# Optimization experiments

Measured on AMD Instinct MI355X. Metric: run time of the kernel, lower is better.

Reference implementation:

```python
import jax, jax.numpy as jnp
import numpy as np

EMB = 512
HEADS = 8
HEAD_DIM = EMB // HEADS


def setup_inputs() -> dict:
    key = jax.random.key(0)
    ks = jax.random.split(key, 9)
    s = 1.0 / np.sqrt(EMB)
    return {
        "x": jax.random.normal(ks[0], (4, 2048, EMB), dtype=jnp.float32),
        "Wq": jax.random.uniform(ks[1], (EMB, EMB), jnp.float32, -s, s),
        "bq": jax.random.uniform(ks[2], (EMB,), jnp.float32, -s, s),
        "Wk": jax.random.uniform(ks[3], (EMB, EMB), jnp.float32, -s, s),
        "bk": jax.random.uniform(ks[4], (EMB,), jnp.float32, -s, s),
        "Wv": jax.random.uniform(ks[5], (EMB, EMB), jnp.float32, -s, s),
        "bv": jax.random.uniform(ks[6], (EMB,), jnp.float32, -s, s),
        "Wp": jax.random.uniform(ks[7], (EMB, EMB), jnp.float32, -s, s),
        "bp": jax.random.uniform(ks[8], (EMB,), jnp.float32, -s, s),
    }


def _split_heads(t):
    b, n, _ = t.shape
    return t.reshape(b, n, HEADS, HEAD_DIM).transpose(0, 2, 1, 3)  # b h n d


def reference(x, Wq, bq, Wk, bk, Wv, bv, Wp, bp):
    q = _split_heads(x @ Wq.T + bq)
    k = _split_heads(x @ Wk.T + bk)
    v = _split_heads(x @ Wv.T + bv)
    energy = jnp.einsum("bhqd,bhkd->bhqk", q, k)
    # NOTE: original applies softmax to UNSCALED logits, then divides probs by sqrt(emb)
    att = jax.nn.softmax(energy, axis=-1) / jnp.sqrt(jnp.float32(EMB))
    out = jnp.einsum("bhqk,bhkd->bhqd", att, v)
    b, h, n, d = out.shape
    out = out.transpose(0, 2, 1, 3).reshape(b, n, h * d)
    return out @ Wp.T + bp
```

## Files before the change

### kernel.cpp

```cpp
#include <hip/hip_runtime.h>
#include <math.h>
#include <stdint.h>

#define SEQ  2048
#define LOG2E 1.4426950408889634f

typedef __attribute__((ext_vector_type(4))) float f32x4;
typedef __attribute__((ext_vector_type(16))) float f32x16;
typedef __attribute__((ext_vector_type(8))) short bf16x8;

template <int V> struct IC { static constexpr int value = V; };

__device__ __forceinline__ unsigned packbf(float a, float b) {
    return __builtin_amdgcn_perm(__float_as_uint(b) + 0x8000u,
                                 __float_as_uint(a) + 0x8000u, 0x07060302u);
}

__global__ __launch_bounds__(256) void cvt_kernel(
    const float* __restrict__ x,  const float* __restrict__ wq,
    const float* __restrict__ wk, const float* __restrict__ wv,
    const float* __restrict__ wp,
    unsigned short* __restrict__ xb,  unsigned short* __restrict__ wqb,
    unsigned short* __restrict__ wkb, unsigned short* __restrict__ wvb,
    unsigned short* __restrict__ wpb)
{
    const int c = blockIdx.x * 256 + threadIdx.x;
    const float* s;
    unsigned short* d;
    int off;
    if (c < 524288) {
        s = x; d = xb; off = c;
    } else {
        const int cc = c - 524288;
        const int wsel = cc >> 15;
        off = cc & 32767;
        s = wsel == 0 ? wq : wsel == 1 ? wk : wsel == 2 ? wv : wp;
        d = wsel == 0 ? wqb : wsel == 1 ? wkb : wsel == 2 ? wvb : wpb;
    }
    const float4* sp = (const float4*)s + (size_t)off * 2;
    const float4 a = sp[0], b = sp[1];
    uint4 p;
    p.x = packbf(a.x, a.y); p.y = packbf(a.z, a.w);
    p.z = packbf(b.x, b.y); p.w = packbf(b.z, b.w);
    *((uint4*)d + off) = p;
}

__global__ __launch_bounds__(256, 3) void qkv_kernel(
    const unsigned short* __restrict__ xb, const unsigned short* __restrict__ wqb,
    const unsigned short* __restrict__ wkb, const unsigned short* __restrict__ wvb,
    const float* __restrict__ bq, const float* __restrict__ bk,
    const float* __restrict__ bv,
    unsigned short* __restrict__ Qw, unsigned short* __restrict__ Kw,
    unsigned short* __restrict__ VTw)
{
    __shared__ __align__(16) unsigned short smem[16384];
    unsigned short* As = smem;
    unsigned short* Bs = smem + 8192;

    const int t = threadIdx.x;
    const int w = t >> 6, lane = t & 63, quad = (t >> 4) & 3, l15 = t & 15;
    const int wr = w >> 1, wc = w & 1;
    const int m0 = blockIdx.y * 128;
    const int n0 = blockIdx.x * 128;
    const int which = n0 >> 9;
    const unsigned short* wbase = which == 0 ? wqb : (which == 1 ? wkb : wvb);
    const int nrow = n0 & 511;

    const int ar = t >> 2, ac = t & 3;
    const unsigned short* ax = xb + (size_t)(m0 + ar) * 512 + ac * 8;
    const unsigned short* bx = wbase + (size_t)(nrow + ar) * 512 + ac * 8;
    const int lws = (ar & 15) | (ac << 4);
    const int off0 = (ar >> 4) * 512 + lws * 8;

    f32x4 acc[4][4];
#pragma unroll
    for (int mt = 0; mt < 4; ++mt)
#pragma unroll
        for (int nt = 0; nt < 4; ++nt) acc[mt][nt] = (f32x4){0.f, 0.f, 0.f, 0.f};

    uint4 ra0, ra1, ra2, ra3, rb0, rb1, rb2, rb3;
    auto loadt = [&](int k0) {
        ra0 = *(const uint4*)(ax + k0);
        ra1 = *(const uint4*)(ax + k0 + 32);
        ra2 = *(const uint4*)(ax + 32768 + k0);
        ra3 = *(const uint4*)(ax + 32768 + k0 + 32);
        rb0 = *(const uint4*)(bx + k0);
        rb1 = *(const uint4*)(bx + k0 + 32);
        rb2 = *(const uint4*)(bx + 32768 + k0);
        rb3 = *(const uint4*)(bx + 32768 + k0 + 32);
    };
    auto writet = [&]() {
        *(uint4*)(As + off0) = ra0;
        *(uint4*)(As + off0 + 4096) = ra1;
        *(uint4*)(As + off0 + 2048) = ra2;
        *(uint4*)(As + off0 + 2048 + 4096) = ra3;
        *(uint4*)(Bs + off0) = rb0;
        *(uint4*)(Bs + off0 + 4096) = rb1;
        *(uint4*)(Bs + off0 + 2048) = rb2;
        *(uint4*)(Bs + off0 + 2048 + 4096) = rb3;
    };

    loadt(0);
    auto kloop = [&](auto TRC) {
        constexpr int TR = decltype(TRC)::value;
        for (int ki = 0; ki < 8; ++ki) {
            writet();
            if (ki < 7) loadt((ki + 1) * 64);
            __syncthreads();
#pragma unroll
            for (int s = 0; s < 2; ++s) {
                bf16x8 af[4], bfr[4];
#pragma unroll
                for (int mt = 0; mt < 4; ++mt)
                    af[mt] = *(const bf16x8*)(As + s * 4096 +
                                              ((wr * 4 + mt) * 64 + lane) * 8);
#pragma unroll
                for (int nt = 0; nt < 4; ++nt)
                    bfr[nt] = *(const bf16x8*)(Bs + s * 4096 +
                                               ((wc * 4 + nt) * 64 + lane) * 8);
#pragma unroll
                for (int mt = 0; mt < 4; ++mt)
#pragma unroll
                    for (int nt = 0; nt < 4; ++nt) {
                        if (TR)
                            acc[mt][nt] = __builtin_amdgcn_mfma_f32_16x16x32_bf16(
                                bfr[nt], af[mt], acc[mt][nt], 0, 0, 0);
                        else
                            acc[mt][nt] = __builtin_amdgcn_mfma_f32_16x16x32_bf16(
                                af[mt], bfr[nt], acc[mt][nt], 0, 0, 0);
                    }
            }
            if (ki < 7) __syncthreads();
        }
    };
    if (which < 2) kloop(IC<1>{});
    else           kloop(IC<0>{});

    if (which == 2) {
#pragma unroll
        for (int nt = 0; nt < 4; ++nt) {
            const int n = n0 + wc * 64 + nt * 16 + l15;
            const float bias = bv[n & 511];
            const int h = (n >> 6) & 7, d = n & 63;
#pragma unroll
            for (int mt = 0; mt < 4; ++mt) {
                const int mb = m0 + wr * 64 + mt * 16 + quad * 4;
                const int bi = mb >> 11, ns = mb & 2047;
                const int bhl = bi * 8 + h;
                const f32x4 v = acc[mt][nt];
                uint2 pk;
                pk.x = packbf(v[0] + bias, v[1] + bias);
                pk.y = packbf(v[2] + bias, v[3] + bias);
                const size_t off =
                    ((size_t)(bhl * 32 + (ns >> 6)) * 8 + ((d >> 5) << 2) +
                     ((ns >> 4) & 3)) * 512 +
                    ((d & 31) << 3) + ((ns & 8) << 5) + (ns & 7);
                *(uint2*)(VTw + off) = pk;
            }
        }
    } else {
        const float sc = which ? 1.f : LOG2E;
        const float* bpt = which ? bk : bq;
        unsigned short* base = which ? Kw : Qw;
#pragma unroll
        for (int nt = 0; nt < 4; ++nt) {
            const int nb = n0 + wc * 64 + nt * 16 + quad * 4;
            const f32x4 bvv = *(const f32x4*)(bpt + (nb & 511));
            const int h = (nb >> 6) & 7, d0 = nb & 63;
#pragma unroll
            for (int mt = 0; mt < 4; ++mt) {
                const int nsg = m0 + wr * 64 + mt * 16 + l15;
                const int bi = nsg >> 11, ns = nsg & 2047;
                const int bhl = bi * 8 + h;
                const f32x4 v = acc[mt][nt];
                uint2 pk;
                pk.x = packbf((v[0] + bvv[0]) * sc, (v[1] + bvv[1]) * sc);
                pk.y = packbf((v[2] + bvv[2]) * sc, (v[3] + bvv[3]) * sc);
                const size_t off =
                    ((size_t)(bhl * 64 + (ns >> 5)) * 4 + (d0 >> 4)) * 512 +
                    ((d0 & 8) << 5) + ((ns & 31) << 3) + (d0 & 7);
                *(uint2*)(base + off) = pk;
            }
        }
    }
}

__global__ __launch_bounds__(256, 3) void outproj_kernel(
    const unsigned short* __restrict__ Aw, const unsigned short* __restrict__ wpb,
    const float* __restrict__ bp, float* __restrict__ out)
{
    __shared__ __align__(16) unsigned short smem[16384];
    unsigned short* As = smem;
    unsigned short* Bs = smem + 8192;

    const int t = threadIdx.x;
    const int w = t >> 6, lane = t & 63, quad = (t >> 4) & 3, l15 = t & 15;
    const int wr = w >> 1, wc = w & 1;
    const int m0 = blockIdx.y * 128;
    const int n0 = blockIdx.x * 128;

    const int ar = t >> 2, ac = t & 3;
    const unsigned short* ap = Aw + (size_t)(m0 + ar) * 512 + ac * 8;
    const unsigned short* bx = wpb + (size_t)(n0 + ar) * 512 + ac * 8;
    const int lws = (ar & 15) | (ac << 4);
    const int off0 = (ar >> 4) * 512 + lws * 8;

    f32x4 acc[4][4];
#pragma unroll
    for (int mt = 0; mt < 4; ++mt)
#pragma unroll
        for (int nt = 0; nt < 4; ++nt) acc[mt][nt] = (f32x4){0.f, 0.f, 0.f, 0.f};

    uint4 ra0, ra1, ra2, ra3, rb0, rb1, rb2, rb3;
    auto loadt = [&](int k0) {
        ra0 = *(const uint4*)(ap + k0);
        ra1 = *(const uint4*)(ap + k0 + 32);
        ra2 = *(const uint4*)(ap + 32768 + k0);
        ra3 = *(const uint4*)(ap + 32768 + k0 + 32);
        rb0 = *(const uint4*)(bx + k0);
        rb1 = *(const uint4*)(bx + k0 + 32);
        rb2 = *(const uint4*)(bx + 32768 + k0);
        rb3 = *(const uint4*)(bx + 32768 + k0 + 32);
    };
    auto writet = [&]() {
        *(uint4*)(As + off0) = ra0;
        *(uint4*)(As + off0 + 4096) = ra1;
        *(uint4*)(As + off0 + 2048) = ra2;
        *(uint4*)(As + off0 + 2048 + 4096) = ra3;
        *(uint4*)(Bs + off0) = rb0;
        *(uint4*)(Bs + off0 + 4096) = rb1;
        *(uint4*)(Bs + off0 + 2048) = rb2;
        *(uint4*)(Bs + off0 + 2048 + 4096) = rb3;
    };

    loadt(0);
    for (int ki = 0; ki < 8; ++ki) {
        writet();
        if (ki < 7) loadt((ki + 1) * 64);
        __syncthreads();
#pragma unroll
        for (int s = 0; s < 2; ++s) {
            bf16x8 af[4], bfr[4];
#pragma unroll
            for (int mt = 0; mt < 4; ++mt)
                af[mt] = *(const bf16x8*)(As + s * 4096 +
                                          ((wr * 4 + mt) * 64 + lane) * 8);
#pragma unroll
            for (int nt = 0; nt < 4; ++nt)
                bfr[nt] = *(const bf16x8*)(Bs + s * 4096 +
                                           ((wc * 4 + nt) * 64 + lane) * 8);
#pragma unroll
            for (int mt = 0; mt < 4; ++mt)
#pragma unroll
                for (int nt = 0; nt < 4; ++nt)
                    acc[mt][nt] = __builtin_amdgcn_mfma_f32_16x16x32_bf16(
                        af[mt], bfr[nt], acc[mt][nt], 0, 0, 0);
        }
        if (ki < 7) __syncthreads();
    }

#pragma unroll
    for (int nt = 0; nt < 4; ++nt) {
        const int n = n0 + wc * 64 + nt * 16 + l15;
        const float bias = bp[n];
#pragma unroll
        for (int mt = 0; mt < 4; ++mt) {
            const int mb = m0 + wr * 64 + mt * 16 + quad * 4;
            const f32x4 v = acc[mt][nt];
#pragma unroll
            for (int r = 0; r < 4; ++r)
                out[(size_t)(mb + r) * 512 + n] = v[r] + bias;
        }
    }
}

#define ATTN_STEP(STC, STN, JT)                                                \
    do {                                                                       \
        const int jt_ = (JT);                                                  \
        bf16x8 vc[4];                                                          \
        _Pragma("unroll")                                                      \
        for (int dg = 0; dg < 2; ++dg)                                         \
            _Pragma("unroll")                                                  \
            for (int p = 0; p < 2; ++p)                                        \
                vc[dg * 2 + p] = *(const bf16x8*)(                             \
                    Vp + (size_t)jt_ * 4096 + (dg * 4 + jh * 2 + p) * 512);    \
        STN = zero;                                                            \
        __builtin_amdgcn_s_setprio(1);                                         \
        _Pragma("unroll")                                                      \
        for (int kt = 0; kt < 4; ++kt)                                         \
            STN = __builtin_amdgcn_mfma_f32_32x32x16_bf16(kc[kt], qf[kt],      \
                                                          STN, 0, 0, 0);       \
        __builtin_amdgcn_s_setprio(0);                                         \
        const int jn_ = (jt_ < 30) ? jt_ + 2 : 31;                             \
        _Pragma("unroll")                                                      \
        for (int c = 0; c < 4; ++c)                                            \
            kc[c] = *(const bf16x8*)(Kp + (size_t)jn_ * 4096 + c * 512);       \
        _Pragma("unroll")                                                      \
        for (int r = 0; r < 16; ++r)                                           \
            STC[r] = __builtin_amdgcn_exp2f(STC[r]);                           \
        {                                                                      \
            float s01 = STC[0] + STC[1],   s23 = STC[2] + STC[3];              \
            float s45 = STC[4] + STC[5],   s67 = STC[6] + STC[7];              \
            float s89 = STC[8] + STC[9],   sAB = STC[10] + STC[11];            \
            float sCD = STC[12] + STC[13], sEF = STC[14] + STC[15];            \
            lpart += ((s01 + s23) + (s45 + s67)) + ((s89 + sAB) + (sCD + sEF));\
        }                                                                      \
        _Pragma("unroll")                                                      \
        for (int p = 0; p < 2; ++p) {                                          \
            const int r0 = p * 8;                                              \
            unsigned a0, a1, b0, b1;                                           \
            asm("v_cvt_pk_bf16_f32 %0, %1, %2"                                 \
                : "=v"(a0) : "v"(STC[r0 + 0]), "v"(STC[r0 + 1]));              \
            asm("v_cvt_pk_bf16_f32 %0, %1, %2"                                 \
                : "=v"(a1) : "v"(STC[r0 + 2]), "v"(STC[r0 + 3]));              \
            asm("v_cvt_pk_bf16_f32 %0, %1, %2"                                 \
                : "=v"(b0) : "v"(STC[r0 + 4]), "v"(STC[r0 + 5]));              \
            asm("v_cvt_pk_bf16_f32 %0, %1, %2"                                 \
                : "=v"(b1) : "v"(STC[r0 + 6]), "v"(STC[r0 + 7]));              \
            asm("v_permlane32_swap_b32 %0, %1" : "+v"(a0), "+v"(b0));          \
            asm("v_permlane32_swap_b32 %0, %1" : "+v"(a1), "+v"(b1));          \
            union { unsigned u[4]; bf16x8 v; } pb;                             \
            pb.u[0] = a0;                                                      \
            pb.u[1] = a1;                                                      \
            pb.u[2] = b0;                                                      \
            pb.u[3] = b1;                                                      \
            __builtin_amdgcn_s_setprio(1);                                     \
            Ot[0] = __builtin_amdgcn_mfma_f32_32x32x16_bf16(vc[0 + p], pb.v,   \
                                                            Ot[0], 0, 0, 0);   \
            Ot[1] = __builtin_amdgcn_mfma_f32_32x32x16_bf16(vc[2 + p], pb.v,   \
                                                            Ot[1], 0, 0, 0);   \
            __builtin_amdgcn_s_setprio(0);                                     \
        }                                                                      \
    } while (0)

__global__ __launch_bounds__(512, 2) void attn_kernel(
    const unsigned short* __restrict__ Qf, const unsigned short* __restrict__ Kf,
    const unsigned short* __restrict__ Vf, unsigned short* __restrict__ Ow)
{
    __shared__ float cb[8448];
    const int t = threadIdx.x;
    const int w = t >> 6, lane = t & 63;
    const int l31 = lane & 31, hlf = lane >> 5;
    const int qi = w >> 1, jh = w & 1;

    if (w & 4) __builtin_amdgcn_s_sleep(15);

    const int bh = blockIdx.x;
    const int qblk = blockIdx.y;
    const int q0 = qblk * 128;

    const unsigned short* Kp = Kf + (size_t)bh * 131072 + (jh * 4) * 512 + lane * 8;
    const unsigned short* Vp = Vf + (size_t)bh * 131072 + lane * 8;

    const int qgg = qblk * 4 + qi;
    const unsigned short* Qp = Qf + ((size_t)(bh * 64 + qgg) * 4) * 512 + lane * 8;
    bf16x8 qf[4];
#pragma unroll
    for (int kt = 0; kt < 4; ++kt)
        qf[kt] = *(const bf16x8*)(Qp + kt * 512);

    f32x16 zero;
#pragma unroll
    for (int r = 0; r < 16; ++r) zero[r] = 0.f;

    float lpart = 0.f;
    f32x16 Ot[2];
    Ot[0] = zero; Ot[1] = zero;

    bf16x8 kc[4];
#pragma unroll
    for (int c = 0; c < 4; ++c)
        kc[c] = *(const bf16x8*)(Kp + c * 512);

    f32x16 stA = zero, stB = zero;
#pragma unroll
    for (int kt = 0; kt < 4; ++kt)
        stA = __builtin_amdgcn_mfma_f32_32x32x16_bf16(kc[kt], qf[kt], stA, 0, 0, 0);
#pragma unroll
    for (int c = 0; c < 4; ++c)
        kc[c] = *(const bf16x8*)(Kp + 4096 + c * 512);

    for (int jt = 0; jt < 32; jt += 2) {
        ATTN_STEP(stA, stB, jt);
        ATTN_STEP(stB, stA, jt + 1);
    }

    if (jh == 1) {
#pragma unroll
        for (int dg = 0; dg < 2; ++dg) {
            const int cidx = (qi * 2 + dg) * 4;
#pragma unroll
            for (int k = 0; k < 4; ++k) {
                float4 v = make_float4(
                    Ot[dg][k * 4 + 0], Ot[dg][k * 4 + 1],
                    Ot[dg][k * 4 + 2], Ot[dg][k * 4 + 3]);
                *(float4*)(cb + (cidx + k) * 256 + lane * 4) = v;
            }
        }
        cb[8192 + qi * 64 + lane] = lpart;
    }
    __syncthreads();
    if (jh == 0) {
        const int bi = bh >> 3, h = bh & 7;
#pragma unroll
        for (int dg = 0; dg < 2; ++dg) {
            const int cidx = (qi * 2 + dg) * 4;
#pragma unroll
            for (int k = 0; k < 4; ++k) {
                const float4 v = *(const float4*)(cb + (cidx + k) * 256 + lane * 4);
                Ot[dg][k * 4 + 0] += v.x;
                Ot[dg][k * 4 + 1] += v.y;
                Ot[dg][k * 4 + 2] += v.z;
                Ot[dg][k * 4 + 3] += v.w;
            }
        }
        float lv = lpart + cb[8192 + qi * 64 + lane];
        lv += __shfl_xor(lv, 32);
        const float inv = 1.0f / (lv * 22.627416997969522f);

        const int ns = q0 + qi * 32 + l31;
        unsigned short* dst = Ow + ((size_t)bi * SEQ + ns) * 512 + h * 64 + hlf * 4;
#pragma unroll
        for (int dg = 0; dg < 2; ++dg)
#pragma unroll
            for (int rb2 = 0; rb2 < 4; ++rb2) {
                uint2 pk;
                pk.x = packbf(Ot[dg][rb2 * 4 + 0] * inv,
                              Ot[dg][rb2 * 4 + 1] * inv);
                pk.y = packbf(Ot[dg][rb2 * 4 + 2] * inv,
                              Ot[dg][rb2 * 4 + 3] * inv);
                *(uint2*)(dst + dg * 32 + rb2 * 8) = pk;
            }
    }
}

extern "C" void kernel_launch(void* const* d_in, const int* in_sizes, int n_in,
                              void* d_out, int out_size, void* d_ws, size_t ws_size,
                              hipStream_t stream)
{
    const float* x  = (const float*)d_in[0];
    const float* Wq = (const float*)d_in[1];
    const float* bq = (const float*)d_in[2];
    const float* Wk = (const float*)d_in[3];
    const float* bk = (const float*)d_in[4];
    const float* Wv = (const float*)d_in[5];
    const float* bv = (const float*)d_in[6];
    const float* Wp = (const float*)d_in[7];
    const float* bp = (const float*)d_in[8];

    unsigned short* ws = (unsigned short*)d_ws;
    unsigned short* Qw  = ws;
    unsigned short* Kw  = Qw + 4194304;
    unsigned short* VTw = Kw + 4194304;
    unsigned short* Owb = VTw + 4194304;
    unsigned short* xb  = Owb;
    unsigned short* wqb = Owb + 4194304;
    unsigned short* wkb = wqb + 262144;
    unsigned short* wvb = wkb + 262144;
    unsigned short* wpb = wvb + 262144;

    cvt_kernel<<<dim3(2560), 256, 0, stream>>>(
        x, Wq, Wk, Wv, Wp, xb, wqb, wkb, wvb, wpb);
    qkv_kernel<<<dim3(12, 64), 256, 0, stream>>>(
        xb, wqb, wkb, wvb, bq, bk, bv, Qw, Kw, VTw);
    attn_kernel<<<dim3(32, 16), 512, 0, stream>>>(Qw, Kw, VTw, Owb);
    outproj_kernel<<<dim3(4, 64), 256, 0, stream>>>(Owb, wpb, bp, (float*)d_out);
}
```

Before: 162.9 us.

## Use direct global-to-LDS loads in QKV GEMM and drop attention wave sleep

The QKV projection now stages A and B tiles with global_load_lds (16-byte direct-to-LDS loads) instead of loading into registers and then writing to shared memory. The K step is halved to 32 and LDS use shrinks to 16KB. The register-prefetch software pipelining is gone, so each iteration now waits on its own load before computing, which exposes load latency. Separately, the s_sleep stagger for the upper waves in the attention kernel is removed.

New measurement: 164.7 us. No clear change (+1.1%).

```diff
diff --git a/kernel.cpp b/kernel.cpp
--- a/kernel.cpp
+++ b/kernel.cpp
@@ -14,6 +14,12 @@
 __device__ __forceinline__ unsigned packbf(float a, float b) {
     return __builtin_amdgcn_perm(__float_as_uint(b) + 0x8000u,
                                  __float_as_uint(a) + 0x8000u, 0x07060302u);
+}
+
+__device__ __forceinline__ void gload16(const unsigned short* g, unsigned short* l) {
+    __builtin_amdgcn_global_load_lds(
+        (const __attribute__((address_space(1))) unsigned int*)g,
+        (__attribute__((address_space(3))) unsigned int*)l, 16, 0, 0);
 }
 
 __global__ __launch_bounds__(256) void cvt_kernel(
@@ -53,9 +59,9 @@
     unsigned short* __restrict__ Qw, unsigned short* __restrict__ Kw,
     unsigned short* __restrict__ VTw)
 {
-    __shared__ __align__(16) unsigned short smem[16384];
+    __shared__ __align__(16) unsigned short smem[8192];
     unsigned short* As = smem;
-    unsigned short* Bs = smem + 8192;
+    unsigned short* Bs = smem + 4096;
 
     const int t = threadIdx.x;
     const int w = t >> 6, lane = t & 63, quad = (t >> 4) & 3, l15 = t & 15;
@@ -66,11 +72,8 @@
     const unsigned short* wbase = which == 0 ? wqb : (which == 1 ? wkb : wvb);
     const int nrow = n0 & 511;
 
-    const int ar = t >> 2, ac = t & 3;
-    const unsigned short* ax = xb + (size_t)(m0 + ar) * 512 + ac * 8;
-    const unsigned short* bx = wbase + (size_t)(nrow + ar) * 512 + ac * 8;
-    const int lws = (ar & 15) | (ac << 4);
-    const int off0 = (ar >> 4) * 512 + lws * 8;
+    const unsigned short* axg = xb + (size_t)(m0 + w * 16 + (lane & 15)) * 512 + ((lane >> 4) * 8);
+    const unsigned short* bxg = wbase + (size_t)(nrow + w * 16 + (lane & 15)) * 512 + ((lane >> 4) * 8);
 
     f32x4 acc[4][4];
 #pragma unroll
@@ -78,59 +81,39 @@
 #pragma unroll
         for (int nt = 0; nt < 4; ++nt) acc[mt][nt] = (f32x4){0.f, 0.f, 0.f, 0.f};
 
-    uint4 ra0, ra1, ra2, ra3, rb0, rb1, rb2, rb3;
-    auto loadt = [&](int k0) {
-        ra0 = *(const uint4*)(ax + k0);
-        ra1 = *(const uint4*)(ax + k0 + 32);
-        ra2 = *(const uint4*)(ax + 32768 + k0);
-        ra3 = *(const uint4*)(ax + 32768 + k0 + 32);
-        rb0 = *(const uint4*)(bx + k0);
-        rb1 = *(const uint4*)(bx + k0 + 32);
-        rb2 = *(const uint4*)(bx + 32768 + k0);
-        rb3 = *(const uint4*)(bx + 32768 + k0 + 32);
+    auto stage = [&](int k0) {
+        unsigned short* Ad = As + w * 512;
+        unsigned short* Bd = Bs + w * 512;
+        gload16(axg + k0, Ad);
+        gload16(axg + 32768 + k0, Ad + 2048);
+        gload16(bxg + k0, Bd);
+        gload16(bxg + 32768 + k0, Bd + 2048);
     };
-    auto writet = [&]() {
-        *(uint4*)(As + off0) = ra0;
-        *(uint4*)(As + off0 + 4096) = ra1;
-        *(uint4*)(As + off0 + 2048) = ra2;
-        *(uint4*)(As + off0 + 2048 + 4096) = ra3;
-        *(uint4*)(Bs + off0) = rb0;
-        *(uint4*)(Bs + off0 + 4096) = rb1;
-        *(uint4*)(Bs + off0 + 2048) = rb2;
-        *(uint4*)(Bs + off0 + 2048 + 4096) = rb3;
-    };
-
-    loadt(0);
+
     auto kloop = [&](auto TRC) {
         constexpr int TR = decltype(TRC)::value;
-        for (int ki = 0; ki < 8; ++ki) {
-            writet();
-            if (ki < 7) loadt((ki + 1) * 64);
+        for (int ki = 0; ki < 16; ++ki) {
+            stage(ki * 32);
             __syncthreads();
-#pragma unroll
-            for (int s = 0; s < 2; ++s) {
-                bf16x8 af[4], bfr[4];
-#pragma unroll
-                for (int mt = 0; mt < 4; ++mt)
-                    af[mt] = *(const bf16x8*)(As + s * 4096 +
-                                              ((wr * 4 + mt) * 64 + lane) * 8);
-#pragma unroll
-                for (int nt = 0; nt < 4; ++nt)
-                    bfr[nt] = *(const bf16x8*)(Bs + s * 4096 +
-                                               ((wc * 4 + nt) * 64 + lane) * 8);
-#pragma unroll
-                for (int mt = 0; mt < 4; ++mt)
-#pragma unroll
-                    for (int nt = 0; nt < 4; ++nt) {
-                        if (TR)
-                            acc[mt][nt] = __builtin_amdgcn_mfma_f32_16x16x32_bf16(
-                                bfr[nt], af[mt], acc[mt][nt], 0, 0, 0);
-                        else
-                            acc[mt][nt] = __builtin_amdgcn_mfma_f32_16x16x32_bf16(
-                                af[mt], bfr[nt], acc[mt][nt], 0, 0, 0);
-                    }
-            }
-            if (ki < 7) __syncthreads();
+            bf16x8 af[4], bfr[4];
+#pragma unroll
+            for (int mt = 0; mt < 4; ++mt)
+                af[mt] = *(const bf16x8*)(As + ((wr * 4 + mt) * 64 + lane) * 8);
+#pragma unroll
+            for (int nt = 0; nt < 4; ++nt)
+                bfr[nt] = *(const bf16x8*)(Bs + ((wc * 4 + nt) * 64 + lane) * 8);
+#pragma unroll
+            for (int mt = 0; mt < 4; ++mt)
+#pragma unroll
+                for (int nt = 0; nt < 4; ++nt) {
+                    if (TR)
+                        acc[mt][nt] = __builtin_amdgcn_mfma_f32_16x16x32_bf16(
+                            bfr[nt], af[mt], acc[mt][nt], 0, 0, 0);
+                    else
+                        acc[mt][nt] = __builtin_amdgcn_mfma_f32_16x16x32_bf16(
+                            af[mt], bfr[nt], acc[mt][nt], 0, 0, 0);
+                }
+            if (ki < 15) __syncthreads();
         }
     };
     if (which < 2) kloop(IC<1>{});
@@ -343,8 +326,6 @@
     const int l31 = lane & 31, hlf = lane >> 5;
     const int qi = w >> 1, jh = w & 1;
 
-    if (w & 4) __builtin_amdgcn_s_sleep(15);
-
     const int bh = blockIdx.x;
     const int qblk = blockIdx.y;
     const int q0 = qblk * 128;
```

## Stage K/V tiles in LDS via async global_load_lds double buffering

Applied to the files above, without the earlier changes.

The attention loop now cooperatively loads each K/V tile into shared memory with global_load_lds into a double buffer, and every wave reads its fragments from LDS. Before, each wave loaded K and V straight from global memory into registers with a software-pipelined ping-pong of score tiles. This shares loads across the waves of a block, which cuts redundant global traffic and drops the staggered-sleep trick. In exchange it adds a block-wide barrier every tile, removes the overlap of the next QK MFMA with the current exp, and reuses the reduction buffer as the K/V staging area.

After: 159.8 us (median of 2 runs). Within noise of the previous version (-1.9%).

```diff
diff --git a/kernel.cpp b/kernel.cpp
--- a/kernel.cpp
+++ b/kernel.cpp
@@ -14,6 +14,12 @@
 __device__ __forceinline__ unsigned packbf(float a, float b) {
     return __builtin_amdgcn_perm(__float_as_uint(b) + 0x8000u,
                                  __float_as_uint(a) + 0x8000u, 0x07060302u);
+}
+
+__device__ __forceinline__ void gload16(const unsigned short* g, unsigned short* l) {
+    __builtin_amdgcn_global_load_lds(
+        (const __attribute__((address_space(1))) unsigned int*)g,
+        (__attribute__((address_space(3))) unsigned int*)l, 16, 0, 0);
 }
 
 __global__ __launch_bounds__(256) void cvt_kernel(
@@ -274,83 +280,24 @@
     }
 }
 
-#define ATTN_STEP(STC, STN, JT)                                                \
-    do {                                                                       \
-        const int jt_ = (JT);                                                  \
-        bf16x8 vc[4];                                                          \
-        _Pragma("unroll")                                                      \
-        for (int dg = 0; dg < 2; ++dg)                                         \
-            _Pragma("unroll")                                                  \
-            for (int p = 0; p < 2; ++p)                                        \
-                vc[dg * 2 + p] = *(const bf16x8*)(                             \
-                    Vp + (size_t)jt_ * 4096 + (dg * 4 + jh * 2 + p) * 512);    \
-        STN = zero;                                                            \
-        __builtin_amdgcn_s_setprio(1);                                         \
-        _Pragma("unroll")                                                      \
-        for (int kt = 0; kt < 4; ++kt)                                         \
-            STN = __builtin_amdgcn_mfma_f32_32x32x16_bf16(kc[kt], qf[kt],      \
-                                                          STN, 0, 0, 0);       \
-        __builtin_amdgcn_s_setprio(0);                                         \
-        const int jn_ = (jt_ < 30) ? jt_ + 2 : 31;                             \
-        _Pragma("unroll")                                                      \
-        for (int c = 0; c < 4; ++c)                                            \
-            kc[c] = *(const bf16x8*)(Kp + (size_t)jn_ * 4096 + c * 512);       \
-        _Pragma("unroll")                                                      \
-        for (int r = 0; r < 16; ++r)                                           \
-            STC[r] = __builtin_amdgcn_exp2f(STC[r]);                           \
-        {                                                                      \
-            float s01 = STC[0] + STC[1],   s23 = STC[2] + STC[3];              \
-            float s45 = STC[4] + STC[5],   s67 = STC[6] + STC[7];              \
-            float s89 = STC[8] + STC[9],   sAB = STC[10] + STC[11];            \
-            float sCD = STC[12] + STC[13], sEF = STC[14] + STC[15];            \
-            lpart += ((s01 + s23) + (s45 + s67)) + ((s89 + sAB) + (sCD + sEF));\
-        }                                                                      \
-        _Pragma("unroll")                                                      \
-        for (int p = 0; p < 2; ++p) {                                          \
-            const int r0 = p * 8;                                              \
-            unsigned a0, a1, b0, b1;                                           \
-            asm("v_cvt_pk_bf16_f32 %0, %1, %2"                                 \
-                : "=v"(a0) : "v"(STC[r0 + 0]), "v"(STC[r0 + 1]));              \
-            asm("v_cvt_pk_bf16_f32 %0, %1, %2"                                 \
-                : "=v"(a1) : "v"(STC[r0 + 2]), "v"(STC[r0 + 3]));              \
-            asm("v_cvt_pk_bf16_f32 %0, %1, %2"                                 \
-                : "=v"(b0) : "v"(STC[r0 + 4]), "v"(STC[r0 + 5]));              \
-            asm("v_cvt_pk_bf16_f32 %0, %1, %2"                                 \
-                : "=v"(b1) : "v"(STC[r0 + 6]), "v"(STC[r0 + 7]));              \
-            asm("v_permlane32_swap_b32 %0, %1" : "+v"(a0), "+v"(b0));          \
-            asm("v_permlane32_swap_b32 %0, %1" : "+v"(a1), "+v"(b1));          \
-            union { unsigned u[4]; bf16x8 v; } pb;                             \
-            pb.u[0] = a0;                                                      \
-            pb.u[1] = a1;                                                      \
-            pb.u[2] = b0;                                                      \
-            pb.u[3] = b1;                                                      \
-            __builtin_amdgcn_s_setprio(1);                                     \
-            Ot[0] = __builtin_amdgcn_mfma_f32_32x32x16_bf16(vc[0 + p], pb.v,   \
-                                                            Ot[0], 0, 0, 0);   \
-            Ot[1] = __builtin_amdgcn_mfma_f32_32x32x16_bf16(vc[2 + p], pb.v,   \
-                                                            Ot[1], 0, 0, 0);   \
-            __builtin_amdgcn_s_setprio(0);                                     \
-        }                                                                      \
-    } while (0)
-
 __global__ __launch_bounds__(512, 2) void attn_kernel(
     const unsigned short* __restrict__ Qf, const unsigned short* __restrict__ Kf,
     const unsigned short* __restrict__ Vf, unsigned short* __restrict__ Ow)
 {
-    __shared__ float cb[8448];
+    __shared__ __align__(16) float cb[8448];
+    unsigned short* kv = (unsigned short*)cb;
+
     const int t = threadIdx.x;
     const int w = t >> 6, lane = t & 63;
     const int l31 = lane & 31, hlf = lane >> 5;
     const int qi = w >> 1, jh = w & 1;
 
-    if (w & 4) __builtin_amdgcn_s_sleep(15);
-
     const int bh = blockIdx.x;
     const int qblk = blockIdx.y;
     const int q0 = qblk * 128;
 
-    const unsigned short* Kp = Kf + (size_t)bh * 131072 + (jh * 4) * 512 + lane * 8;
-    const unsigned short* Vp = Vf + (size_t)bh * 131072 + lane * 8;
+    const unsigned short* Kt = Kf + (size_t)bh * 131072;
+    const unsigned short* Vt = Vf + (size_t)bh * 131072;
 
     const int qgg = qblk * 4 + qi;
     const unsigned short* Qp = Qf + ((size_t)(bh * 64 + qgg) * 4) * 512 + lane * 8;
@@ -367,22 +314,76 @@
     f32x16 Ot[2];
     Ot[0] = zero; Ot[1] = zero;
 
-    bf16x8 kc[4];
-#pragma unroll
-    for (int c = 0; c < 4; ++c)
-        kc[c] = *(const bf16x8*)(Kp + c * 512);
-
-    f32x16 stA = zero, stB = zero;
-#pragma unroll
-    for (int kt = 0; kt < 4; ++kt)
-        stA = __builtin_amdgcn_mfma_f32_32x32x16_bf16(kc[kt], qf[kt], stA, 0, 0, 0);
-#pragma unroll
-    for (int c = 0; c < 4; ++c)
-        kc[c] = *(const bf16x8*)(Kp + 4096 + c * 512);
-
-    for (int jt = 0; jt < 32; jt += 2) {
-        ATTN_STEP(stA, stB, jt);
-        ATTN_STEP(stB, stA, jt + 1);
+    auto stage = [&](int b, int jt) {
+        unsigned short* dst = kv + b * 8192 + w * 512;
+        gload16(Kt + (size_t)jt * 4096 + w * 512 + lane * 8, dst);
+        gload16(Vt + (size_t)jt * 4096 + w * 512 + lane * 8, dst + 4096);
+    };
+
+    stage(0, 0);
+    __syncthreads();
+    int cur = 0;
+
+    for (int jt = 0; jt < 32; ++jt) {
+        if (jt < 31) stage(cur ^ 1, jt + 1);
+
+        const unsigned short* kb = kv + cur * 8192;
+        bf16x8 kc[4], vc[4];
+#pragma unroll
+        for (int c = 0; c < 4; ++c)
+            kc[c] = *(const bf16x8*)(kb + (jh * 4 + c) * 512 + lane * 8);
+#pragma unroll
+        for (int dg = 0; dg < 2; ++dg)
+#pragma unroll
+            for (int p = 0; p < 2; ++p)
+                vc[dg * 2 + p] = *(const bf16x8*)(
+                    kb + 4096 + (dg * 4 + jh * 2 + p) * 512 + lane * 8);
+
+        f32x16 st = zero;
+        __builtin_amdgcn_s_setprio(1);
+#pragma unroll
+        for (int kt = 0; kt < 4; ++kt)
+            st = __builtin_amdgcn_mfma_f32_32x32x16_bf16(kc[kt], qf[kt], st, 0, 0, 0);
+        __builtin_amdgcn_s_setprio(0);
+
+#pragma unroll
+        for (int r = 0; r < 16; ++r)
+            st[r] = __builtin_amdgcn_exp2f(st[r]);
+        {
+            float s01 = st[0] + st[1],   s23 = st[2] + st[3];
+            float s45 = st[4] + st[5],   s67 = st[6] + st[7];
+            float s89 = st[8] + st[9],   sAB = st[10] + st[11];
+            float sCD = st[12] + st[13], sEF = st[14] + st[15];
+            lpart += ((s01 + s23) + (s45 + s67)) + ((s89 + sAB) + (sCD + sEF));
+        }
+
+#pragma unroll
+        for (int p = 0; p < 2; ++p) {
+            const int r0 = p * 8;
+            unsigned a0, a1, b0, b1;
+            asm("v_cvt_pk_bf16_f32 %0, %1, %2"
+                : "=v"(a0) : "v"(st[r0 + 0]), "v"(st[r0 + 1]));
+            asm("v_cvt_pk_bf16_f32 %0, %1, %2"
+                : "=v"(a1) : "v"(st[r0 + 2]), "v"(st[r0 + 3]));
+            asm("v_cvt_pk_bf16_f32 %0, %1, %2"
+                : "=v"(b0) : "v"(st[r0 + 4]), "v"(st[r0 + 5]));
+            asm("v_cvt_pk_bf16_f32 %0, %1, %2"
+                : "=v"(b1) : "v"(st[r0 + 6]), "v"(st[r0 + 7]));
+            asm("v_permlane32_swap_b32 %0, %1" : "+v"(a0), "+v"(b0));
+            asm("v_permlane32_swap_b32 %0, %1" : "+v"(a1), "+v"(b1));
+            union { unsigned u[4]; bf16x8 v; } pb;
+            pb.u[0] = a0;
+            pb.u[1] = a1;
+            pb.u[2] = b0;
+            pb.u[3] = b1;
+            __builtin_amdgcn_s_setprio(1);
+            Ot[0] = __builtin_amdgcn_mfma_f32_32x32x16_bf16(vc[0 + p], pb.v, Ot[0], 0, 0, 0);
+            Ot[1] = __builtin_amdgcn_mfma_f32_32x32x16_bf16(vc[2 + p], pb.v, Ot[1], 0, 0, 0);
+            __builtin_amdgcn_s_setprio(0);
+        }
+
+        __syncthreads();
+        cur ^= 1;
     }
 
     if (jh == 1) {
```

## Stage K/V tiles into LDS via async global_load_lds double buffering

Applied to the files above, without the earlier changes.

Replaces per-wave direct global loads of K and V fragments with cooperative asynchronous global-to-LDS copies into a double-buffered shared tile, two key tiles per iteration. All eight waves share each staged tile instead of every wave fetching its own K/V from global or L2, which cuts redundant global traffic. The software-pipelined QK/softmax interleave and the staggered s_sleep for half the waves are removed. The change adds a __syncthreads per iteration and 64KB of LDS per block, which may limit occupancy at two blocks per CU.

Result: no change. 160.9 us (-1.2%).

```diff
diff --git a/kernel.cpp b/kernel.cpp
--- a/kernel.cpp
+++ b/kernel.cpp
@@ -14,6 +14,12 @@
 __device__ __forceinline__ unsigned packbf(float a, float b) {
     return __builtin_amdgcn_perm(__float_as_uint(b) + 0x8000u,
                                  __float_as_uint(a) + 0x8000u, 0x07060302u);
+}
+
+__device__ __forceinline__ void gload16(const unsigned short* g, unsigned short* l) {
+    __builtin_amdgcn_global_load_lds(
+        (const __attribute__((address_space(1))) unsigned int*)g,
+        (__attribute__((address_space(3))) unsigned int*)l, 16, 0, 0);
 }
 
 __global__ __launch_bounds__(256) void cvt_kernel(
@@ -274,35 +280,23 @@
     }
 }
 
-#define ATTN_STEP(STC, STN, JT)                                                \
+#define ATTN_FINISH(ST, KB)                                                    \
     do {                                                                       \
-        const int jt_ = (JT);                                                  \
         bf16x8 vc[4];                                                          \
         _Pragma("unroll")                                                      \
         for (int dg = 0; dg < 2; ++dg)                                         \
             _Pragma("unroll")                                                  \
             for (int p = 0; p < 2; ++p)                                        \
                 vc[dg * 2 + p] = *(const bf16x8*)(                             \
-                    Vp + (size_t)jt_ * 4096 + (dg * 4 + jh * 2 + p) * 512);    \
-        STN = zero;                                                            \
-        __builtin_amdgcn_s_setprio(1);                                         \
-        _Pragma("unroll")                                                      \
-        for (int kt = 0; kt < 4; ++kt)                                         \
-            STN = __builtin_amdgcn_mfma_f32_32x32x16_bf16(kc[kt], qf[kt],      \
-                                                          STN, 0, 0, 0);       \
-        __builtin_amdgcn_s_setprio(0);                                         \
-        const int jn_ = (jt_ < 30) ? jt_ + 2 : 31;                             \
-        _Pragma("unroll")                                                      \
-        for (int c = 0; c < 4; ++c)                                            \
-            kc[c] = *(const bf16x8*)(Kp + (size_t)jn_ * 4096 + c * 512);       \
+                    (KB) + 4096 + (dg * 4 + jh * 2 + p) * 512 + lane * 8);     \
         _Pragma("unroll")                                                      \
         for (int r = 0; r < 16; ++r)                                           \
-            STC[r] = __builtin_amdgcn_exp2f(STC[r]);                           \
+            ST[r] = __builtin_amdgcn_exp2f(ST[r]);                             \
         {                                                                      \
-            float s01 = STC[0] + STC[1],   s23 = STC[2] + STC[3];              \
-            float s45 = STC[4] + STC[5],   s67 = STC[6] + STC[7];              \
-            float s89 = STC[8] + STC[9],   sAB = STC[10] + STC[11];            \
-            float sCD = STC[12] + STC[13], sEF = STC[14] + STC[15];            \
+            float s01 = ST[0] + ST[1],   s23 = ST[2] + ST[3];                  \
+            float s45 = ST[4] + ST[5],   s67 = ST[6] + ST[7];                  \
+            float s89 = ST[8] + ST[9],   sAB = ST[10] + ST[11];                \
+            float sCD = ST[12] + ST[13], sEF = ST[14] + ST[15];                \
             lpart += ((s01 + s23) + (s45 + s67)) + ((s89 + sAB) + (sCD + sEF));\
         }                                                                      \
         _Pragma("unroll")                                                      \
@@ -310,13 +304,13 @@
             const int r0 = p * 8;                                              \
             unsigned a0, a1, b0, b1;                                           \
             asm("v_cvt_pk_bf16_f32 %0, %1, %2"                                 \
-                : "=v"(a0) : "v"(STC[r0 + 0]), "v"(STC[r0 + 1]));              \
+                : "=v"(a0) : "v"(ST[r0 + 0]), "v"(ST[r0 + 1]));                \
             asm("v_cvt_pk_bf16_f32 %0, %1, %2"                                 \
-                : "=v"(a1) : "v"(STC[r0 + 2]), "v"(STC[r0 + 3]));              \
+                : "=v"(a1) : "v"(ST[r0 + 2]), "v"(ST[r0 + 3]));                \
             asm("v_cvt_pk_bf16_f32 %0, %1, %2"                                 \
-                : "=v"(b0) : "v"(STC[r0 + 4]), "v"(STC[r0 + 5]));              \
+                : "=v"(b0) : "v"(ST[r0 + 4]), "v"(ST[r0 + 5]));                \
             asm("v_cvt_pk_bf16_f32 %0, %1, %2"                                 \
-                : "=v"(b1) : "v"(STC[r0 + 6]), "v"(STC[r0 + 7]));              \
+                : "=v"(b1) : "v"(ST[r0 + 6]), "v"(ST[r0 + 7]));                \
             asm("v_permlane32_swap_b32 %0, %1" : "+v"(a0), "+v"(b0));          \
             asm("v_permlane32_swap_b32 %0, %1" : "+v"(a1), "+v"(b1));          \
             union { unsigned u[4]; bf16x8 v; } pb;                             \
@@ -337,20 +331,21 @@
     const unsigned short* __restrict__ Qf, const unsigned short* __restrict__ Kf,
     const unsigned short* __restrict__ Vf, unsigned short* __restrict__ Ow)
 {
-    __shared__ float cb[8448];
+    __shared__ __align__(16) unsigned short kvs[32768];
+    unsigned short* kv = kvs;
+    float* cb = (float*)kvs;
+
     const int t = threadIdx.x;
     const int w = t >> 6, lane = t & 63;
     const int l31 = lane & 31, hlf = lane >> 5;
     const int qi = w >> 1, jh = w & 1;
 
-    if (w & 4) __builtin_amdgcn_s_sleep(15);
-
     const int bh = blockIdx.x;
     const int qblk = blockIdx.y;
     const int q0 = qblk * 128;
 
-    const unsigned short* Kp = Kf + (size_t)bh * 131072 + (jh * 4) * 512 + lane * 8;
-    const unsigned short* Vp = Vf + (size_t)bh * 131072 + lane * 8;
+    const unsigned short* Kt = Kf + (size_t)bh * 131072;
+    const unsigned short* Vt = Vf + (size_t)bh * 131072;
 
     const int qgg = qblk * 4 + qi;
     const unsigned short* Qp = Qf + ((size_t)(bh * 64 + qgg) * 4) * 512 + lane * 8;
@@ -367,22 +362,49 @@
     f32x16 Ot[2];
     Ot[0] = zero; Ot[1] = zero;
 
-    bf16x8 kc[4];
-#pragma unroll
-    for (int c = 0; c < 4; ++c)
-        kc[c] = *(const bf16x8*)(Kp + c * 512);
-
-    f32x16 stA = zero, stB = zero;
-#pragma unroll
-    for (int kt = 0; kt < 4; ++kt)
-        stA = __builtin_amdgcn_mfma_f32_32x32x16_bf16(kc[kt], qf[kt], stA, 0, 0, 0);
-#pragma unroll
-    for (int c = 0; c < 4; ++c)
-        kc[c] = *(const bf16x8*)(Kp + 4096 + c * 512);
-
-    for (int jt = 0; jt < 32; jt += 2) {
-        ATTN_STEP(stA, stB, jt);
-        ATTN_STEP(stB, stA, jt + 1);
+    auto stage = [&](int b, int slot, int jt) {
+        unsigned short* dst = kv + b * 16384 + slot * 8192 + w * 512;
+        gload16(Kt + (size_t)jt * 4096 + w * 512 + lane * 8, dst);
+        gload16(Vt + (size_t)jt * 4096 + w * 512 + lane * 8, dst + 4096);
+    };
+
+    stage(0, 0, 0);
+    stage(0, 1, 1);
+    __syncthreads();
+    int cur = 0;
+
+    for (int it = 0; it < 16; ++it) {
+        if (it < 15) {
+            stage(cur ^ 1, 0, 2 * it + 2);
+            stage(cur ^ 1, 1, 2 * it + 3);
+        }
+
+        const unsigned short* kb0 = kv + cur * 16384;
+        const unsigned short* kb1 = kb0 + 8192;
+
+        bf16x8 kc0[4], kc1[4];
+#pragma unroll
+        for (int c = 0; c < 4; ++c)
+            kc0[c] = *(const bf16x8*)(kb0 + (jh * 4 + c) * 512 + lane * 8);
+#pragma unroll
+        for (int c = 0; c < 4; ++c)
+            kc1[c] = *(const bf16x8*)(kb1 + (jh * 4 + c) * 512 + lane * 8);
+
+        f32x16 st0 = zero, st1 = zero;
+        __builtin_amdgcn_s_setprio(1);
+#pragma unroll
+        for (int kt = 0; kt < 4; ++kt)
+            st0 = __builtin_amdgcn_mfma_f32_32x32x16_bf16(kc0[kt], qf[kt], st0, 0, 0, 0);
+#pragma unroll
+        for (int kt = 0; kt < 4; ++kt)
+            st1 = __builtin_amdgcn_mfma_f32_32x32x16_bf16(kc1[kt], qf[kt], st1, 0, 0, 0);
+        __builtin_amdgcn_s_setprio(0);
+
+        ATTN_FINISH(st0, kb0);
+        ATTN_FINISH(st1, kb1);
+
+        __syncthreads();
+        cur ^= 1;
     }
 
     if (jh == 1) {
```
